# Kernel tuning notes

Hardware: AMD Instinct MI355X
Metric: run time of the kernel (lower is better)

The kernel has to match this reference:

```python
import jax, jax.numpy as jnp
import numpy as np

EPS_BN = 1e-5
EPS_LN = 1e-5
OUT_H, OUT_W = 256, 256


def conv2d(x, w, b, pad):
    y = jax.lax.conv_general_dilated(x, w, (1, 1), [(pad, pad), (pad, pad)],
                                     dimension_numbers=('NCHW', 'OIHW', 'NCHW'))
    return y + b[None, :, None, None]


def leaky(x):
    return jnp.where(x >= 0, x, 0.2 * x)


def bn_eval(x, g, b):
    # fresh BatchNorm2d in eval mode: running_mean=0, running_var=1
    scale = g / jnp.sqrt(1.0 + EPS_BN)
    return x * scale[None, :, None, None] + b[None, :, None, None]


def resize_bilinear(x, oh, ow):
    # align_corners=True bilinear, separable gathers
    n, c, h, w = x.shape
    sy = jnp.arange(oh, dtype=x.dtype) * ((h - 1) / (oh - 1))
    sx = jnp.arange(ow, dtype=x.dtype) * ((w - 1) / (ow - 1))
    y0 = jnp.clip(jnp.floor(sy).astype(jnp.int32), 0, h - 2)
    x0 = jnp.clip(jnp.floor(sx).astype(jnp.int32), 0, w - 2)
    fy = (sy - y0.astype(x.dtype))[None, None, :, None]
    fx = (sx - x0.astype(x.dtype))[None, None, None, :]
    top = x[:, :, y0, :] * (1 - fy) + x[:, :, y0 + 1, :] * fy        # (n,c,oh,w)
    out = top[:, :, :, x0] * (1 - fx) + top[:, :, :, x0 + 1] * fx    # (n,c,oh,ow)
    return out


def layernorm(x, g, b):
    mu = jnp.mean(x, axis=-1, keepdims=True)
    var = jnp.mean((x - mu) ** 2, axis=-1, keepdims=True)
    return (x - mu) * jax.lax.rsqrt(var + EPS_LN) * g + b


def setup_inputs() -> dict:
    key = jax.random.key(0)
    ks = iter(jax.random.split(key, 64))

    def rn(shape, scale=0.05):
        return (jax.random.normal(next(ks), shape, dtype=jnp.float32) * scale)

    inp = {'x': jax.random.normal(next(ks), (8, 64, 128, 128), dtype=jnp.float32)}
    inp.update(
        r_c7a_w=rn((16, 64, 7, 7)), r_c7a_b=jnp.zeros((16,), jnp.float32),
        r_c1_w=rn((16, 16, 1, 1)), r_c1_b=jnp.zeros((16,), jnp.float32),
        r_bn1_g=1.0 + rn((16,), 0.1), r_bn1_b=jnp.zeros((16,), jnp.float32),
        rb_c1_w=rn((16, 16, 3, 3)), rb_c1_b=jnp.zeros((16,), jnp.float32),
        rb_bn1_g=1.0 + rn((16,), 0.1), rb_bn1_b=jnp.zeros((16,), jnp.float32),
        rb_c2_w=rn((16, 16, 3, 3)), rb_c2_b=jnp.zeros((16,), jnp.float32),
        rb_bn2_g=1.0 + rn((16,), 0.1), rb_bn2_b=jnp.zeros((16,), jnp.float32),
        r_c3_w=rn((16, 16, 3, 3)), r_c3_b=jnp.zeros((16,), jnp.float32),
        r_bn2_g=1.0 + rn((16,), 0.1), r_bn2_b=jnp.zeros((16,), jnp.float32),
        r_c7b_w=rn((64, 16, 7, 7)), r_c7b_b=jnp.zeros((64,), jnp.float32),
        a_k_w=rn((1, 64, 1, 1)), a_k_b=jnp.zeros((1,), jnp.float32),
        a_q_w=rn((1, 64, 1, 1)), a_q_b=jnp.zeros((1,), jnp.float32),
        a_v_w=rn((8, 64, 1, 1)), a_v_b=jnp.zeros((8,), jnp.float32),
        a_r_w=rn((64, 8, 1, 1)), a_r_b=jnp.zeros((64,), jnp.float32),
        t_ln_g=jnp.ones((64,), jnp.float32), t_ln_b=jnp.zeros((64,), jnp.float32),
        t_fc1_w=rn((64, 64)), t_fc1_b=jnp.zeros((64,), jnp.float32),
        t_fc2_w=rn((64, 64)), t_fc2_b=jnp.zeros((64,), jnp.float32),
    )
    return inp


def reference(x, r_c7a_w, r_c7a_b, r_c1_w, r_c1_b, r_bn1_g, r_bn1_b,
              rb_c1_w, rb_c1_b, rb_bn1_g, rb_bn1_b, rb_c2_w, rb_c2_b,
              rb_bn2_g, rb_bn2_b, r_c3_w, r_c3_b, r_bn2_g, r_bn2_b,
              r_c7b_w, r_c7b_b, a_k_w, a_k_b, a_q_w, a_q_b, a_v_w, a_v_b,
              a_r_w, a_r_b, t_ln_g, t_ln_b, t_fc1_w, t_fc1_b, t_fc2_w, t_fc2_b):
    # ---- Resizer ----
    identity = resize_bilinear(x, OUT_H, OUT_W)
    y = leaky(conv2d(x, r_c7a_w, r_c7a_b, 3))
    y = bn_eval(leaky(conv2d(y, r_c1_w, r_c1_b, 0)), r_bn1_g, r_bn1_b)
    y = resize_bilinear(y, OUT_H, OUT_W)
    conv_identity = y
    z = leaky(bn_eval(conv2d(y, rb_c1_w, rb_c1_b, 1), rb_bn1_g, rb_bn1_b))
    z = bn_eval(conv2d(z, rb_c2_w, rb_c2_b, 1), rb_bn2_g, rb_bn2_b) + y
    z = bn_eval(conv2d(z, r_c3_w, r_c3_b, 1), r_bn2_g, r_bn2_b) + conv_identity
    out = conv2d(z, r_c7b_w, r_c7b_b, 3) + identity

    # ---- EfficientAttention (key_channels=1, head_count=1, value_channels=8) ----
    n, c, h, w = out.shape
    hw = h * w
    k = conv2d(out, a_k_w, a_k_b, 0).reshape(n, 1, hw)
    q = conv2d(out, a_q_w, a_q_b, 0).reshape(n, 1, hw)
    v = conv2d(out, a_v_w, a_v_b, 0).reshape(n, 8, hw)
    key = jax.nn.softmax(k, axis=2)            # softmax over spatial positions
    query = jax.nn.softmax(q, axis=1)          # size-1 channel axis -> ones (faithful)
    context = jnp.einsum('nkp,nvp->nkv', key, v)          # (n,1,8)
    att = jnp.einsum('nkv,nkp->nvp', context, query)      # (n,8,hw)
    out = conv2d(att.reshape(n, 8, h, w), a_r_w, a_r_b, 0) + out

    # ---- TransformerBlock (identity conv, 1 encoder: x + MLP(LN(x))) ----
    t = out.reshape(n, c, hw).transpose(2, 0, 1)          # (hw, n, c)
    tn = layernorm(t, t_ln_g, t_ln_b)
    m = jax.nn.gelu(tn @ t_fc1_w.T + t_fc1_b, approximate=False) @ t_fc2_w.T + t_fc2_b
    t = t + m
    return t.transpose(1, 2, 0).reshape(n, c, h, w)
```

## Files before the change

kernel.cpp:

```cpp
#include <hip/hip_runtime.h>
#include <math.h>

#define DI __device__ __forceinline__
#define HW128 (128*128)
#define HW256 (256*256)

__device__ const float BN_RS = 0.9999950000374997f;

DI float leakyf(float x){ return x >= 0.f ? x : 0.2f*x; }

DI unsigned short f2bf(float f){
    unsigned u = __float_as_uint(f);
    return (unsigned short)((u + 0x7fffu + ((u >> 16) & 1u)) >> 16);
}
DI void unpack2(unsigned u, float& lo, float& hi){
    lo = __uint_as_float(u << 16);
    hi = __uint_as_float(u & 0xffff0000u);
}
DI void load8(const uint4* s, size_t idx, unsigned* d){
    uint4 t0 = s[idx], t1 = s[idx + 1];
    d[0]=t0.x; d[1]=t0.y; d[2]=t0.z; d[3]=t0.w;
    d[4]=t1.x; d[5]=t1.y; d[6]=t1.z; d[7]=t1.w;
}

typedef __attribute__((ext_vector_type(8))) short short8v;
typedef __attribute__((ext_vector_type(4))) float float4v;

__global__ __launch_bounds__(256) void prepack(
    const float* __restrict__ w7a, const float* __restrict__ w1,
    const float* __restrict__ w3a, const float* __restrict__ b3a, const float* __restrict__ g3a, const float* __restrict__ be3a,
    const float* __restrict__ w3b, const float* __restrict__ b3b, const float* __restrict__ g3b, const float* __restrict__ be3b,
    const float* __restrict__ w3c, const float* __restrict__ b3c, const float* __restrict__ g3c, const float* __restrict__ be3c,
    const float* __restrict__ w7b, const float* __restrict__ fc1w, const float* __restrict__ fc2w,
    unsigned short* __restrict__ p7aB, float* __restrict__ p1,
    float* __restrict__ q3a, float* __restrict__ q3b, float* __restrict__ q3c,
    unsigned short* __restrict__ w3aB, unsigned short* __restrict__ w3bB, unsigned short* __restrict__ w3cB,
    unsigned short* __restrict__ pwB,
    unsigned short* __restrict__ pwT1, unsigned short* __restrict__ pwT2)
{
    int i = blockIdx.x * 256 + threadIdx.x;
    if (i < 57344) {
        int g = i / 14336, rem = i - g*14336;
        int ks = rem >> 9, oc = (rem >> 5) & 15, k = rem & 31;
        int ky = ks >> 2, kx = ((ks & 3) << 1) + (k >> 4), ic = g*16 + (k & 15);
        p7aB[i] = (kx < 7) ? f2bf(w7a[(oc*64 + ic)*49 + ky*7 + kx]) : (unsigned short)0;
    }
    if (i < 57344) {
        int ks = i >> 11, oc = (i >> 5) & 63, k = i & 31;
        int ky = ks >> 2, kx = ((ks & 3) << 1) + (k >> 4), ic = k & 15;
        pwB[i] = (kx < 7) ? f2bf(w7b[((oc*16 + ic)*7 + ky)*7 + kx]) : (unsigned short)0;
    }
    if (i < 3072) {
        int ks = i >> 9, oc = (i >> 5) & 15, k = i & 31;
        int ky = ks >> 1, kx = ((ks & 1) << 1) + (k >> 4), ic = k & 15;
        if (kx < 3) {
            int src = (oc*16 + ic)*9 + ky*3 + kx;
            w3aB[i] = f2bf(w3a[src] * (g3a[oc]*BN_RS));
            w3bB[i] = f2bf(w3b[src] * (g3b[oc]*BN_RS));
            w3cB[i] = f2bf(w3c[src] * (g3c[oc]*BN_RS));
        } else {
            w3aB[i] = 0; w3bB[i] = 0; w3cB[i] = 0;
        }
    }
    if (i < 256) { int oc = i & 15, ic = i >> 4; p1[i] = w1[oc*16 + ic]; }
    if (i < 16) {
        q3a[i] = b3a[i]*(g3a[i]*BN_RS) + be3a[i];
        q3b[i] = b3b[i]*(g3b[i]*BN_RS) + be3b[i];
        q3c[i] = b3c[i]*(g3c[i]*BN_RS) + be3c[i];
    }
    if (i < 4096) { pwT1[i] = f2bf(fc1w[i]); pwT2[i] = f2bf(fc2w[i]); }
}

__global__ __launch_bounds__(256) void x_to_ci(
    const float* __restrict__ x, unsigned short* __restrict__ xci)
{
    int idx = blockIdx.x*256 + threadIdx.x;
    int p = idx & 16383, gn = idx >> 14;
    int g = gn & 3, n = gn >> 2;
    const float* xb = x + (size_t)(n*64 + g*16)*HW128 + p;
    unsigned q[8];
#pragma unroll
    for (int h = 0; h < 8; ++h) {
        float a0 = xb[(size_t)(2*h)*HW128];
        float a1 = xb[(size_t)(2*h + 1)*HW128];
        q[h] = (unsigned)f2bf(a0) | ((unsigned)f2bf(a1) << 16);
    }
    uint4* dst = (uint4*)xci + (size_t)idx*2;
    dst[0] = make_uint4(q[0], q[1], q[2], q[3]);
    dst[1] = make_uint4(q[4], q[5], q[6], q[7]);
}

__global__ __launch_bounds__(256) void conv7a_mfma(
    const unsigned short* __restrict__ xci,
    const unsigned short* __restrict__ pw,
    const float* __restrict__ b7a, const float* __restrict__ p1,
    const float* __restrict__ b1, const float* __restrict__ bng,
    const float* __restrict__ bnb, unsigned short* __restrict__ y2ci)
{
    __shared__ __align__(16) unsigned char lds[17408];
    unsigned short* tile = (unsigned short*)lds;
    float* P16 = (float*)lds;

    const int tid = threadIdx.x;
    const int n = blockIdx.z, ox = blockIdx.x*16, oy = blockIdx.y*16;
    const int w = tid >> 6, l = tid & 63, lg = l >> 4, ln = l & 15;

    float4v acc[4];
#pragma unroll
    for (int mi = 0; mi < 4; ++mi) acc[mi] = (float4v){0.f,0.f,0.f,0.f};

    const uint4* xc4 = (const uint4*)xci;
    uint4* tl4 = (uint4*)tile;
    const short8v* Bb = (const short8v*)pw;

    for (int g = 0; g < 4; ++g) {
        __syncthreads();
        for (int u = tid; u < 1056; u += 256) {
            int r = u / 48, s = u - r*48;
            int y = oy + r - 3, xcol = ox + (s >> 1) - 3;
            uint4 v = make_uint4(0u,0u,0u,0u);
            if (y >= 0 && y < 128 && xcol >= 0 && xcol < 128)
                v = xc4[((size_t)(n*4 + g)*16384 + y*128 + xcol)*2 + (s & 1)];
            tl4[u] = v;
        }
        __syncthreads();
        for (int ks = 0; ks < 28; ++ks) {
            const int ky = ks >> 2, kxp = (ks & 3) << 1;
            short8v b = Bb[(g*28 + ks)*64 + ln*4 + lg];
            short8v a[4];
#pragma unroll
            for (int mi = 0; mi < 4; ++mi) {
                int row = (4*w + mi) + ky;
                a[mi] = *(const short8v*)(tile + (row*24 + ln + kxp)*16 + lg*8);
            }
#pragma unroll
            for (int mi = 0; mi < 4; ++mi)
                acc[mi] = __builtin_amdgcn_mfma_f32_16x16x32_bf16(a[mi], b, acc[mi], 0, 0, 0);
        }
    }
    __syncthreads();
    const float bo = b7a[ln];
#pragma unroll
    for (int mi = 0; mi < 4; ++mi)
#pragma unroll
        for (int r = 0; r < 4; ++r)
            P16[((4*w + mi)*16 + lg*4 + r)*17 + ln] = leakyf(acc[mi][r] + bo);
    __syncthreads();
    const int py = tid >> 4, pxx = tid & 15;
    float lv[16];
#pragma unroll
    for (int ic = 0; ic < 16; ++ic) lv[ic] = P16[tid*17 + ic];
    float u16[16];
#pragma unroll
    for (int o = 0; o < 16; ++o) {
        float u = b1[o];
#pragma unroll
        for (int ic = 0; ic < 16; ++ic) u += lv[ic] * p1[ic*16 + o];
        u = leakyf(u);
        u16[o] = u * (bng[o]*BN_RS) + bnb[o];
    }
    const int p = (oy + py)*128 + ox + pxx;
    unsigned q[8];
#pragma unroll
    for (int h = 0; h < 8; ++h)
        q[h] = (unsigned)f2bf(u16[2*h]) | ((unsigned)f2bf(u16[2*h+1]) << 16);
    uint4* dst = (uint4*)y2ci + (size_t)(n*16384 + p)*2;
    dst[0] = make_uint4(q[0], q[1], q[2], q[3]);
    dst[1] = make_uint4(q[4], q[5], q[6], q[7]);
}

__global__ __launch_bounds__(256) void resize_ci(
    const unsigned short* __restrict__ y2ci, unsigned short* __restrict__ yci)
{
    const int n = blockIdx.z;
    const int ox = blockIdx.x*16 + threadIdx.x;
    const int oy = blockIdx.y*16 + threadIdx.y;
    float sy = oy * (127.f/255.f), sx = ox * (127.f/255.f);
    int y0 = min((int)sy, 126), x0 = min((int)sx, 126);
    float fy = sy - y0, fx = sx - x0;
    const uint4* src = (const uint4*)y2ci;
    size_t i00 = ((size_t)n*16384 + y0*128 + x0)*2;
    unsigned A00[8], A01[8], A10[8], A11[8];
    load8(src, i00,       A00);
    load8(src, i00 + 2,   A01);
    load8(src, i00 + 256, A10);
    load8(src, i00 + 258, A11);
    unsigned q[8];
#pragma unroll
    for (int h = 0; h < 8; ++h) {
        float l00, h00, l01, h01, l10, h10, l11, h11;
        unpack2(A00[h], l00, h00); unpack2(A01[h], l01, h01);
        unpack2(A10[h], l10, h10); unpack2(A11[h], l11, h11);
        float lo = (l00*(1.f-fx) + l01*fx)*(1.f-fy) + (l10*(1.f-fx) + l11*fx)*fy;
        float hi = (h00*(1.f-fx) + h01*fx)*(1.f-fy) + (h10*(1.f-fx) + h11*fx)*fy;
        q[h] = (unsigned)f2bf(lo) | ((unsigned)f2bf(hi) << 16);
    }
    uint4* dst = (uint4*)yci + ((size_t)n*65536 + oy*256 + ox)*2;
    dst[0] = make_uint4(q[0], q[1], q[2], q[3]);
    dst[1] = make_uint4(q[4], q[5], q[6], q[7]);
}

template<int MODE>
__global__ __launch_bounds__(256) void conv3_mfma(
    const unsigned short* __restrict__ in_ci,
    const unsigned short* __restrict__ wB, const float* __restrict__ q3,
    const unsigned short* __restrict__ res_ci,
    unsigned short* __restrict__ out_ci)
{
    __shared__ __align__(16) unsigned char lds[17408];
    unsigned short* tile = (unsigned short*)lds;
    float* P16 = (float*)lds;

    const int tid = threadIdx.x;
    const int n = blockIdx.z, ox = blockIdx.x*16, oy = blockIdx.y*16;
    const int w = tid >> 6, l = tid & 63, lg = l >> 4, ln = l & 15;

    const uint4* zc = (const uint4*)in_ci;
    uint4* tl4 = (uint4*)tile;
    for (int u = tid; u < 720; u += 256) {
        int r = u / 40, s = u - r*40;
        int y = oy + r - 1, xcol = ox + (s >> 1) - 1;
        uint4 v = make_uint4(0u,0u,0u,0u);
        if (y >= 0 && y < 256 && xcol >= 0 && xcol < 256)
            v = zc[((size_t)n*65536 + y*256 + xcol)*2 + (s & 1)];
        tl4[u] = v;
    }
    __syncthreads();

    float4v acc[4];
#pragma unroll
    for (int mi = 0; mi < 4; ++mi) acc[mi] = (float4v){0.f,0.f,0.f,0.f};
    const short8v* Bb = (const short8v*)wB;
#pragma unroll
    for (int ks = 0; ks < 6; ++ks) {
        const int ky = ks >> 1, kxp = (ks & 1) << 1;
        short8v b = Bb[(ks*16 + ln)*4 + lg];
        short8v a[4];
#pragma unroll
        for (int mi = 0; mi < 4; ++mi) {
            int row = (4*w + mi) + ky;
            a[mi] = *(const short8v*)(tile + (row*20 + ln + kxp)*16 + lg*8);
        }
#pragma unroll
        for (int mi = 0; mi < 4; ++mi)
            acc[mi] = __builtin_amdgcn_mfma_f32_16x16x32_bf16(a[mi], b, acc[mi], 0, 0, 0);
    }
    __syncthreads();
#pragma unroll
    for (int mi = 0; mi < 4; ++mi)
#pragma unroll
        for (int r = 0; r < 4; ++r)
            P16[((4*w + mi)*16 + lg*4 + r)*17 + ln] = acc[mi][r];
    __syncthreads();

    const int py = tid >> 4, pxx = tid & 15;
    const int p = (oy + py)*256 + ox + pxx;
    float u16[16];
#pragma unroll
    for (int o = 0; o < 16; ++o) u16[o] = P16[tid*17 + o] + q3[o];
    if (MODE == 0) {
#pragma unroll
        for (int o = 0; o < 16; ++o) u16[o] = leakyf(u16[o]);
    } else {
        unsigned R[8];
        load8((const uint4*)res_ci, ((size_t)n*65536 + p)*2, R);
#pragma unroll
        for (int h = 0; h < 8; ++h) {
            float lo, hi; unpack2(R[h], lo, hi);
            u16[2*h] += lo; u16[2*h+1] += hi;
        }
    }
    unsigned q[8];
#pragma unroll
    for (int h = 0; h < 8; ++h)
        q[h] = (unsigned)f2bf(u16[2*h]) | ((unsigned)f2bf(u16[2*h+1]) << 16);
    uint4* dst = (uint4*)out_ci + ((size_t)n*65536 + p)*2;
    dst[0] = make_uint4(q[0], q[1], q[2], q[3]);
    dst[1] = make_uint4(q[4], q[5], q[6], q[7]);
}

__global__ __launch_bounds__(256) void conv7b_mfma(
    const unsigned short* __restrict__ z_ci,
    const unsigned short* __restrict__ pwB,
    const unsigned short* __restrict__ xci,
    const float* __restrict__ bias,
    const float* __restrict__ akw, const float* __restrict__ akb,
    float* __restrict__ out0, float* __restrict__ kbuf)
{
    __shared__ __align__(16) unsigned char lds[17408 + 14400];
    unsigned short* tile = (unsigned short*)lds;
    float* P16 = (float*)lds;
    unsigned short* xt16 = (unsigned short*)(lds + 17408);

    const int tid = threadIdx.x;
    const int n = blockIdx.z, ox = blockIdx.x*16, oy = blockIdx.y*16;
    const float SC = 127.f/255.f;
    const int ybase = (int)(oy*SC), xbase = (int)(ox*SC);

    const uint4* zc = (const uint4*)z_ci;
    uint4* tl4 = (uint4*)tile;
    for (int u = tid; u < 1056; u += 256) {
        int r = u / 48, s = u - r*48;
        int y = oy + r - 3, xcol = ox + (s >> 1) - 3;
        uint4 v = make_uint4(0u, 0u, 0u, 0u);
        if (y >= 0 && y < 256 && xcol >= 0 && xcol < 256)
            v = zc[(size_t)((n*256 + y)*256 + xcol)*2 + (s & 1)];
        tl4[u] = v;
    }
    const uint4* xc4 = (const uint4*)xci;
    uint4* xt4 = (uint4*)xt16;
    for (int u = tid; u < 900; u += 256) {
        int p = u / 9, s = u - p*9;
        uint4 v = make_uint4(0u, 0u, 0u, 0u);
        if (s < 8) {
            int g = s >> 1, half = s & 1;
            int r = p / 10, c = p - r*10;
            int y = ybase + r, xcc = xbase + c;
            if (y < 128 && xcc < 128)
                v = xc4[((size_t)(n*4 + g)*16384 + y*128 + xcc)*2 + half];
        }
        xt4[u] = v;
    }
    __syncthreads();

    const int w = tid >> 6, l = tid & 63;
    const int lg = l >> 4, ln = l & 15;
    float4v acc[4][4];
#pragma unroll
    for (int mi = 0; mi < 4; ++mi)
#pragma unroll
        for (int nt = 0; nt < 4; ++nt)
            acc[mi][nt] = (float4v){0.f, 0.f, 0.f, 0.f};

    const short8v* Bb = (const short8v*)pwB;
    for (int ks = 0; ks < 28; ++ks) {
        const int ky = ks >> 2, kxp = (ks & 3) << 1;
        short8v a[4], b[4];
#pragma unroll
        for (int mi = 0; mi < 4; ++mi) {
            int row = (4*w + mi) + ky;
            a[mi] = *(const short8v*)(tile + (row*24 + ln + kxp)*16 + lg*8);
        }
#pragma unroll
        for (int nt = 0; nt < 4; ++nt)
            b[nt] = Bb[ks*256 + nt*64 + ln*4 + lg];
#pragma unroll
        for (int mi = 0; mi < 4; ++mi)
#pragma unroll
            for (int nt = 0; nt < 4; ++nt)
                acc[mi][nt] = __builtin_amdgcn_mfma_f32_16x16x32_bf16(
                    a[mi], b[nt], acc[mi][nt], 0, 0, 0);
    }

    const int py = tid >> 4, pxx = tid & 15;
    const int ohy = oy + py, ohx = ox + pxx;
    float sy = ohy*SC, sx = ohx*SC;
    int y0 = min((int)sy, 126), x0 = min((int)sx, 126);
    float fy = sy - y0, fx = sx - x0;
    const int ly = y0 - ybase, lx = x0 - xbase;
    const int p = ohy*256 + ohx;
    const uint4* xt4c = (const uint4*)xt16;
    const size_t q00 = (size_t)(ly*10 + lx)*9;
    float kacc = akb[0];

    for (int nt = 0; nt < 4; ++nt) {
        __syncthreads();
#pragma unroll
        for (int mi = 0; mi < 4; ++mi)
#pragma unroll
            for (int r = 0; r < 4; ++r)
                P16[((4*w + mi)*16 + lg*4 + r)*17 + ln] = acc[mi][nt][r];
        __syncthreads();
        unsigned A00[8], A01[8], A10[8], A11[8];
        size_t qb = q00 + nt*2;
        load8(xt4c, qb,      A00);
        load8(xt4c, qb + 9,  A01);
        load8(xt4c, qb + 90, A10);
        load8(xt4c, qb + 99, A11);
        float u16[16];
#pragma unroll
        for (int h = 0; h < 8; ++h) {
            float l00, h00, l01, h01, l10, h10, l11, h11;
            unpack2(A00[h], l00, h00); unpack2(A01[h], l01, h01);
            unpack2(A10[h], l10, h10); unpack2(A11[h], l11, h11);
            u16[2*h]   = (l00*(1.f-fx) + l01*fx)*(1.f-fy) + (l10*(1.f-fx) + l11*fx)*fy;
            u16[2*h+1] = (h00*(1.f-fx) + h01*fx)*(1.f-fy) + (h10*(1.f-fx) + h11*fx)*fy;
        }
#pragma unroll
        for (int o = 0; o < 16; ++o) {
            int oc = nt*16 + o;
            float u = P16[tid*17 + o] + bias[oc] + u16[o];
            out0[(size_t)(n*64 + oc)*HW256 + p] = u;
            kacc += akw[oc] * u;
        }
    }
    kbuf[n*65536 + p] = kacc;
}

__global__ __launch_bounds__(256) void softmax_part(
    const float* __restrict__ kb, float* __restrict__ pst)
{
    __shared__ float red[4];
    __shared__ float bcast;
    const int pc = blockIdx.x, n = blockIdx.y, tid = threadIdx.x;
    const float* kp = kb + n*65536 + pc*8192;
    float mx = -3.0e38f;
    for (int i = tid; i < 8192; i += 256) mx = fmaxf(mx, kp[i]);
#pragma unroll
    for (int off = 1; off < 64; off <<= 1) mx = fmaxf(mx, __shfl_xor(mx, off));
    int w = tid >> 6, l = tid & 63;
    if (l == 0) red[w] = mx;
    __syncthreads();
    if (tid == 0) bcast = fmaxf(fmaxf(red[0], red[1]), fmaxf(red[2], red[3]));
    __syncthreads();
    float BM = bcast;
    float s = 0.f;
    for (int i = tid; i < 8192; i += 256) s += __expf(kp[i] - BM);
#pragma unroll
    for (int off = 1; off < 64; off <<= 1) s += __shfl_xor(s, off);
    __syncthreads();
    if (l == 0) red[w] = s;
    __syncthreads();
    if (tid == 0) {
        pst[(n*8 + pc)*2]     = BM;
        pst[(n*8 + pc)*2 + 1] = red[0] + red[1] + red[2] + red[3];
    }
}

__global__ __launch_bounds__(64) void softmax_comb(
    const float* __restrict__ pst, float* __restrict__ st)
{
    int tid = threadIdx.x;
    if (tid < 8) {
        int n = tid;
        float MX = -3.0e38f;
        for (int c = 0; c < 8; ++c) MX = fmaxf(MX, pst[(n*8 + c)*2]);
        float S = 0.f;
        for (int c = 0; c < 8; ++c)
            S += pst[(n*8 + c)*2 + 1] * __expf(pst[(n*8 + c)*2] - MX);
        st[n] = MX; st[8 + n] = 1.f / S;
    }
}

__global__ __launch_bounds__(256) void att_wsum(
    const float* __restrict__ out0, const float* __restrict__ kb,
    const float* __restrict__ st, float* __restrict__ Sp)
{
    const int cg = blockIdx.x, pc = blockIdx.y, n = blockIdx.z, c0 = cg*8;
    const float mx = st[n];
    const float* kp = kb + n*65536 + pc*16384;
    const float* base = out0 + (size_t)(n*64 + c0)*HW256 + pc*16384;
    float acc[8];
#pragma unroll
    for (int c = 0; c < 8; ++c) acc[c] = 0.f;
    for (int p = threadIdx.x; p < 16384; p += 256) {
        float e = __expf(kp[p] - mx);
#pragma unroll
        for (int c = 0; c < 8; ++c) acc[c] += e * base[c*HW256 + p];
    }
#pragma unroll
    for (int c = 0; c < 8; ++c)
#pragma unroll
        for (int off = 1; off < 64; off <<= 1) acc[c] += __shfl_xor(acc[c], off);
    __shared__ float red[4][8];
    int w = threadIdx.x >> 6, l = threadIdx.x & 63;
    if (l == 0) {
#pragma unroll
        for (int c = 0; c < 8; ++c) red[w][c] = acc[c];
    }
    __syncthreads();
    if (threadIdx.x < 8)
        Sp[n*256 + pc*64 + c0 + threadIdx.x] =
            red[0][threadIdx.x] + red[1][threadIdx.x] + red[2][threadIdx.x] + red[3][threadIdx.x];
}

__global__ __launch_bounds__(512) void ctx_addc(
    const float* __restrict__ Sp, const float* __restrict__ st,
    const float* __restrict__ avw, const float* __restrict__ avb,
    const float* __restrict__ arw, const float* __restrict__ arb,
    float* __restrict__ addc)
{
    __shared__ float ctx[8][8];
    const int tid = threadIdx.x;
    if (tid < 64) {
        int n = tid >> 3, vc = tid & 7;
        float s = 0.f;
        for (int c = 0; c < 64; ++c) {
            float Sv = Sp[n*256 + c] + Sp[n*256 + 64 + c]
                     + Sp[n*256 + 128 + c] + Sp[n*256 + 192 + c];
            s += avw[vc*64 + c] * Sv;
        }
        ctx[n][vc] = s * st[8 + n] + avb[vc];
    }
    __syncthreads();
    int n = tid >> 6, c = tid & 63;
    float a = arb[c];
#pragma unroll
    for (int vc = 0; vc < 8; ++vc) a += arw[c*8 + vc] * ctx[n][vc];
    addc[n*64 + c] = a;
}

__global__ __launch_bounds__(256) void transformer_mfma(
    float* __restrict__ out0, const float* __restrict__ addc,
    const float* __restrict__ lng, const float* __restrict__ lnb,
    const unsigned short* __restrict__ W1b, const float* __restrict__ fc1b,
    const unsigned short* __restrict__ W2b, const float* __restrict__ fc2b)
{
    __shared__ __align__(16) unsigned char lds[17408 + 9216 + 2048];
    float*          Xt = (float*)lds;
    unsigned short* Xb = (unsigned short*)(lds + 17408);
    unsigned short* Hb = Xb;
    float* ps  = (float*)(lds + 17408 + 9216);
    float* ps2 = ps + 256;

    const int tid = threadIdx.x;
    const int n = blockIdx.x >> 10;
    const int p0 = (blockIdx.x & 1023) << 6;
    const float* ac = addc + n*64;

#pragma unroll
    for (int k = 0; k < 4; ++k) {
        int v = k*256 + tid;
        int c = v >> 4, i4 = (v & 15) << 2;
        float4v q = *(const float4v*)(out0 + (size_t)(n*64 + c)*HW256 + p0 + i4);
        float a = ac[c];
#pragma unroll
        for (int r = 0; r < 4; ++r) q[r] += a;
        *(float4v*)&Xt[c*68 + i4] = q;
    }
    __syncthreads();

    const int token = tid & 63, q = tid >> 6;
    float t16[16];
    {
        float sum = 0.f, sq = 0.f;
#pragma unroll
        for (int e = 0; e < 16; ++e) {
            float v = Xt[(q*16 + e)*68 + token];
            t16[e] = v; sum += v; sq += v*v;
        }
        ps[q*64 + token] = sum; ps2[q*64 + token] = sq;
    }
    __syncthreads();
    {
        float sum = ps[token] + ps[64 + token] + ps[128 + token] + ps[192 + token];
        float sq  = ps2[token] + ps2[64 + token] + ps2[128 + token] + ps2[192 + token];
        float mu = sum * (1.f/64.f);
        float var = fmaxf(sq * (1.f/64.f) - mu*mu, 0.f);
        float rs = rsqrtf(var + 1e-5f);
#pragma unroll
        for (int c8 = 0; c8 < 2; ++c8) {
            short8v pk;
#pragma unroll
            for (int e = 0; e < 8; ++e) {
                int c = q*16 + c8*8 + e;
                pk[e] = (short)f2bf((t16[c8*8 + e] - mu)*rs*lng[c] + lnb[c]);
            }
            *(short8v*)&Xb[token*72 + q*16 + c8*8] = pk;
        }
    }
    __syncthreads();

    const int w = tid >> 6, l = tid & 63, lg = l >> 4, ln = l & 15;

    float4v acc1[4];
#pragma unroll
    for (int nt = 0; nt < 4; ++nt) acc1[nt] = (float4v){0.f,0.f,0.f,0.f};
#pragma unroll
    for (int kk = 0; kk < 2; ++kk) {
        short8v a = *(const short8v*)&Xb[(w*16 + ln)*72 + kk*32 + lg*8];
        short8v b[4];
#pragma unroll
        for (int nt = 0; nt < 4; ++nt)
            b[nt] = *(const short8v*)&W1b[(nt*16 + ln)*64 + kk*32 + lg*8];
#pragma unroll
        for (int nt = 0; nt < 4; ++nt)
            acc1[nt] = __builtin_amdgcn_mfma_f32_16x16x32_bf16(a, b[nt], acc1[nt], 0, 0, 0);
    }
    __syncthreads();
#pragma unroll
    for (int nt = 0; nt < 4; ++nt) {
        int j = nt*16 + ln;
        float bj = fc1b[j];
#pragma unroll
        for (int r = 0; r < 4; ++r) {
            int tok = w*16 + lg*4 + r;
            float m = acc1[nt][r] + bj;
            float g = 0.5f*m*(1.f + erff(m*0.70710678118654752f));
            Hb[tok*72 + j] = f2bf(g);
        }
    }
    __syncthreads();

    float4v acc2[4];
#pragma unroll
    for (int nt = 0; nt < 4; ++nt) acc2[nt] = (float4v){0.f,0.f,0.f,0.f};
#pragma unroll
    for (int kk = 0; kk < 2; ++kk) {
        short8v a = *(const short8v*)&Hb[(w*16 + ln)*72 + kk*32 + lg*8];
        short8v b[4];
#pragma unroll
        for (int nt = 0; nt < 4; ++nt)
            b[nt] = *(const short8v*)&W2b[(nt*16 + ln)*64 + kk*32 + lg*8];
#pragma unroll
        for (int nt = 0; nt < 4; ++nt)
            acc2[nt] = __builtin_amdgcn_mfma_f32_16x16x32_bf16(a, b[nt], acc2[nt], 0, 0, 0);
    }
#pragma unroll
    for (int nt = 0; nt < 4; ++nt) {
        int c = nt*16 + ln;
        int tb = w*16 + lg*4;
        float add = fc2b[c];
        float4v t4 = *(const float4v*)&Xt[c*68 + tb];
        float* dst = out0 + (size_t)(n*64 + c)*HW256 + p0 + tb;
        float4v o;
#pragma unroll
        for (int r = 0; r < 4; ++r) o[r] = t4[r] + acc2[nt][r] + add;
        *(float4v*)dst = o;
    }
}

extern "C" void kernel_launch(void* const* d_in, const int* in_sizes, int n_in,
                              void* d_out, int out_size, void* d_ws, size_t ws_size,
                              hipStream_t stream)
{
    (void)in_sizes; (void)n_in; (void)out_size; (void)ws_size;
    const float* x    = (const float*)d_in[0];
    const float* w7a  = (const float*)d_in[1];
    const float* b7a  = (const float*)d_in[2];
    const float* w1   = (const float*)d_in[3];
    const float* b1   = (const float*)d_in[4];
    const float* g1   = (const float*)d_in[5];
    const float* be1  = (const float*)d_in[6];
    const float* w3a  = (const float*)d_in[7];
    const float* b3a  = (const float*)d_in[8];
    const float* g3a  = (const float*)d_in[9];
    const float* be3a = (const float*)d_in[10];
    const float* w3b  = (const float*)d_in[11];
    const float* b3b  = (const float*)d_in[12];
    const float* g3b  = (const float*)d_in[13];
    const float* be3b = (const float*)d_in[14];
    const float* w3c  = (const float*)d_in[15];
    const float* b3c  = (const float*)d_in[16];
    const float* g3c  = (const float*)d_in[17];
    const float* be3c = (const float*)d_in[18];
    const float* w7b  = (const float*)d_in[19];
    const float* b7b  = (const float*)d_in[20];
    const float* akw  = (const float*)d_in[21];
    const float* akb  = (const float*)d_in[22];
    const float* avw  = (const float*)d_in[25];
    const float* avb  = (const float*)d_in[26];
    const float* arw  = (const float*)d_in[27];
    const float* arb  = (const float*)d_in[28];
    const float* lng  = (const float*)d_in[29];
    const float* lnb  = (const float*)d_in[30];
    const float* fc1w = (const float*)d_in[31];
    const float* fc1b = (const float*)d_in[32];
    const float* fc2w = (const float*)d_in[33];
    const float* fc2b = (const float*)d_in[34];

    float* ws = (float*)d_ws;
    unsigned short* y2ci = (unsigned short*)ws;
    unsigned short* yci  = (unsigned short*)(ws + 1048576);
    unsigned short* z1ci = (unsigned short*)(ws + 1048576 + 4194304);
    unsigned short* z2ci = (unsigned short*)(ws + 1048576 + 2*4194304);
    unsigned short* xci  = (unsigned short*)(ws + 1048576 + 3*4194304);
    float* o_k   = ws + 1048576 + 4*4194304;
    float* o_st  = o_k + 524288;
    float* o_pst = o_st + 64;
    float* o_Sp  = o_pst + 128;
    float* o_ad  = o_Sp + 2048;
    unsigned short* p7aB = (unsigned short*)(o_ad + 512);
    float* p1   = o_ad + 512 + 28672;
    float* q3a  = p1 + 256;
    float* q3b  = q3a + 16;
    float* q3c  = q3b + 16;
    unsigned short* w3aB = (unsigned short*)(q3c + 16);
    unsigned short* w3bB = w3aB + 3072;
    unsigned short* w3cB = w3bB + 3072;
    unsigned short* pwB  = w3cB + 3072;
    unsigned short* pwT1 = pwB + 57344;
    unsigned short* pwT2 = pwT1 + 4096;

    unsigned short* z3ci = z1ci;
    float* out0 = (float*)d_out;

    prepack<<<224, 256, 0, stream>>>(w7a, w1, w3a,b3a,g3a,be3a, w3b,b3b,g3b,be3b,
                                     w3c,b3c,g3c,be3c, w7b, fc1w, fc2w,
                                     p7aB, p1, q3a, q3b, q3c, w3aB, w3bB, w3cB,
                                     pwB, pwT1, pwT2);
    x_to_ci<<<2048, 256, 0, stream>>>(x, xci);
    conv7a_mfma<<<dim3(8,8,8), 256, 0, stream>>>(xci, p7aB, b7a, p1, b1, g1, be1, y2ci);
    resize_ci<<<dim3(16,16,8), dim3(16,16), 0, stream>>>(y2ci, yci);
    conv3_mfma<0><<<dim3(16,16,8), 256, 0, stream>>>(yci,  w3aB, q3a, nullptr, z1ci);
    conv3_mfma<1><<<dim3(16,16,8), 256, 0, stream>>>(z1ci, w3bB, q3b, yci,     z2ci);
    conv3_mfma<1><<<dim3(16,16,8), 256, 0, stream>>>(z2ci, w3cB, q3c, yci,     z3ci);
    conv7b_mfma<<<dim3(16,16,8), 256, 0, stream>>>(z3ci, pwB, xci, b7b, akw, akb, out0, o_k);
    softmax_part<<<dim3(8,8), 256, 0, stream>>>(o_k, o_pst);
    softmax_comb<<<1, 64, 0, stream>>>(o_pst, o_st);
    att_wsum<<<dim3(8,4,8), 256, 0, stream>>>(out0, o_k, o_st, o_Sp);
    ctx_addc<<<1, 512, 0, stream>>>(o_Sp, o_st, avw, avb, arw, arb, o_ad);
    transformer_mfma<<<8192, 256, 0, stream>>>(out0, o_ad, lng, lnb, pwT1, fc1b, pwT2, fc2b);
}
```

Baseline: 325.2 us.

## Store conv7b output as bf16 channel-interleaved intermediate for attention and transformer

conv7b now writes its output as packed bf16 in a per-pixel channel-interleaved layout instead of fp32 NCHW into the final output buffer. att_wsum is reorganised to read this layout, with each thread covering 16 channels over pixel chunks, and ctx_addc gains a reduction over the larger partial-sum array. The transformer kernel loads bf16 tokens into a smaller LDS tile and writes fp32 to the output once. This removes an fp32 write plus two fp32 reads of the 134 MB intermediate, at the cost of bf16 rounding on the residual path.

```diff
diff --git a/kernel.cpp b/kernel.cpp
--- a/kernel.cpp
+++ b/kernel.cpp
@@ -13,6 +13,7 @@
     unsigned u = __float_as_uint(f);
     return (unsigned short)((u + 0x7fffu + ((u >> 16) & 1u)) >> 16);
 }
+DI float bf2f(unsigned short us){ return __uint_as_float((unsigned)us << 16); }
 DI void unpack2(unsigned u, float& lo, float& hi){
     lo = __uint_as_float(u << 16);
     hi = __uint_as_float(u & 0xffff0000u);
@@ -285,7 +286,7 @@
     const unsigned short* __restrict__ xci,
     const float* __restrict__ bias,
     const float* __restrict__ akw, const float* __restrict__ akb,
-    float* __restrict__ out0, float* __restrict__ kbuf)
+    unsigned short* __restrict__ oci, float* __restrict__ kbuf)
 {
     __shared__ __align__(16) unsigned char lds[17408 + 14400];
     unsigned short* tile = (unsigned short*)lds;
@@ -362,6 +363,7 @@
     const uint4* xt4c = (const uint4*)xt16;
     const size_t q00 = (size_t)(ly*10 + lx)*9;
     float kacc = akb[0];
+    uint4* odst = (uint4*)oci + ((size_t)(n*65536 + p))*8;
 
     for (int nt = 0; nt < 4; ++nt) {
         __syncthreads();
@@ -386,13 +388,18 @@
             u16[2*h]   = (l00*(1.f-fx) + l01*fx)*(1.f-fy) + (l10*(1.f-fx) + l11*fx)*fy;
             u16[2*h+1] = (h00*(1.f-fx) + h01*fx)*(1.f-fy) + (h10*(1.f-fx) + h11*fx)*fy;
         }
+        unsigned qpk[8];
 #pragma unroll
         for (int o = 0; o < 16; ++o) {
             int oc = nt*16 + o;
-            float u = P16[tid*17 + o] + bias[oc] + u16[o];
-            out0[(size_t)(n*64 + oc)*HW256 + p] = u;
-            kacc += akw[oc] * u;
-        }
+            u16[o] = P16[tid*17 + o] + bias[oc] + u16[o];
+            kacc += akw[oc] * u16[o];
+        }
+#pragma unroll
+        for (int h = 0; h < 8; ++h)
+            qpk[h] = (unsigned)f2bf(u16[2*h]) | ((unsigned)f2bf(u16[2*h+1]) << 16);
+        odst[nt*2]     = make_uint4(qpk[0], qpk[1], qpk[2], qpk[3]);
+        odst[nt*2 + 1] = make_uint4(qpk[4], qpk[5], qpk[6], qpk[7]);
     }
     kbuf[n*65536 + p] = kacc;
 }
@@ -443,35 +450,46 @@
 }
 
 __global__ __launch_bounds__(256) void att_wsum(
-    const float* __restrict__ out0, const float* __restrict__ kb,
+    const unsigned short* __restrict__ oci, const float* __restrict__ kb,
     const float* __restrict__ st, float* __restrict__ Sp)
 {
-    const int cg = blockIdx.x, pc = blockIdx.y, n = blockIdx.z, c0 = cg*8;
+    const int pc = blockIdx.x, n = blockIdx.y, tid = threadIdx.x;
+    const int qr = tid & 3, pidx0 = tid >> 2;
     const float mx = st[n];
-    const float* kp = kb + n*65536 + pc*16384;
-    const float* base = out0 + (size_t)(n*64 + c0)*HW256 + pc*16384;
-    float acc[8];
-#pragma unroll
-    for (int c = 0; c < 8; ++c) acc[c] = 0.f;
-    for (int p = threadIdx.x; p < 16384; p += 256) {
+    float acc[16];
+#pragma unroll
+    for (int c = 0; c < 16; ++c) acc[c] = 0.f;
+    const float* kp = kb + n*65536 + pc*2048;
+    const uint4* base = (const uint4*)oci + ((size_t)(n*65536 + pc*2048))*8 + qr*2;
+    for (int p = pidx0; p < 2048; p += 64) {
         float e = __expf(kp[p] - mx);
-#pragma unroll
-        for (int c = 0; c < 8; ++c) acc[c] += e * base[c*HW256 + p];
-    }
-#pragma unroll
-    for (int c = 0; c < 8; ++c)
-#pragma unroll
-        for (int off = 1; off < 64; off <<= 1) acc[c] += __shfl_xor(acc[c], off);
-    __shared__ float red[4][8];
-    int w = threadIdx.x >> 6, l = threadIdx.x & 63;
-    if (l == 0) {
-#pragma unroll
-        for (int c = 0; c < 8; ++c) red[w][c] = acc[c];
-    }
-    __syncthreads();
-    if (threadIdx.x < 8)
-        Sp[n*256 + pc*64 + c0 + threadIdx.x] =
-            red[0][threadIdx.x] + red[1][threadIdx.x] + red[2][threadIdx.x] + red[3][threadIdx.x];
+        uint4 t0 = base[(size_t)p*8], t1 = base[(size_t)p*8 + 1];
+        unsigned d[8] = {t0.x, t0.y, t0.z, t0.w, t1.x, t1.y, t1.z, t1.w};
+#pragma unroll
+        for (int h = 0; h < 8; ++h) {
+            float lo, hi; unpack2(d[h], lo, hi);
+            acc[2*h] += e*lo; acc[2*h + 1] += e*hi;
+        }
+    }
+#pragma unroll
+    for (int c = 0; c < 16; ++c) {
+        acc[c] += __shfl_xor(acc[c], 4);
+        acc[c] += __shfl_xor(acc[c], 8);
+        acc[c] += __shfl_xor(acc[c], 16);
+        acc[c] += __shfl_xor(acc[c], 32);
+    }
+    __shared__ float red[4][4][16];
+    int w = tid >> 6, l = tid & 63;
+    if (l < 4) {
+#pragma unroll
+        for (int c = 0; c < 16; ++c) red[w][l][c] = acc[c];
+    }
+    __syncthreads();
+    if (tid < 64) {
+        int q2 = tid >> 4, c = tid & 15;
+        Sp[n*2048 + pc*64 + q2*16 + c] =
+            red[0][q2][c] + red[1][q2][c] + red[2][q2][c] + red[3][q2][c];
+    }
 }
 
 __global__ __launch_bounds__(512) void ctx_addc(
@@ -480,16 +498,20 @@
     const float* __restrict__ arw, const float* __restrict__ arb,
     float* __restrict__ addc)
 {
+    __shared__ float Sf[512];
     __shared__ float ctx[8][8];
     const int tid = threadIdx.x;
+    {
+        int n = tid >> 6, c = tid & 63;
+        float s = 0.f;
+        for (int k = 0; k < 32; ++k) s += Sp[n*2048 + k*64 + c];
+        Sf[n*64 + c] = s;
+    }
+    __syncthreads();
     if (tid < 64) {
         int n = tid >> 3, vc = tid & 7;
         float s = 0.f;
-        for (int c = 0; c < 64; ++c) {
-            float Sv = Sp[n*256 + c] + Sp[n*256 + 64 + c]
-                     + Sp[n*256 + 128 + c] + Sp[n*256 + 192 + c];
-            s += avw[vc*64 + c] * Sv;
-        }
+        for (int c = 0; c < 64; ++c) s += avw[vc*64 + c] * Sf[n*64 + c];
         ctx[n][vc] = s * st[8 + n] + avb[vc];
     }
     __syncthreads();
@@ -501,32 +523,35 @@
 }
 
 __global__ __launch_bounds__(256) void transformer_mfma(
-    float* __restrict__ out0, const float* __restrict__ addc,
+    const unsigned short* __restrict__ oci, float* __restrict__ out,
+    const float* __restrict__ addc,
     const float* __restrict__ lng, const float* __restrict__ lnb,
     const unsigned short* __restrict__ W1b, const float* __restrict__ fc1b,
     const unsigned short* __restrict__ W2b, const float* __restrict__ fc2b)
 {
-    __shared__ __align__(16) unsigned char lds[17408 + 9216 + 2048];
-    float*          Xt = (float*)lds;
-    unsigned short* Xb = (unsigned short*)(lds + 17408);
+    __shared__ __align__(16) unsigned char lds[8448 + 9216 + 2048 + 256];
+    unsigned* Xci = (unsigned*)lds;
+    unsigned short* Xcis = (unsigned short*)lds;
+    unsigned short* Xb = (unsigned short*)(lds + 8448);
     unsigned short* Hb = Xb;
-    float* ps  = (float*)(lds + 17408 + 9216);
+    float* ps  = (float*)(lds + 8448 + 9216);
     float* ps2 = ps + 256;
+    float* ach = ps2 + 256;
 
     const int tid = threadIdx.x;
     const int n = blockIdx.x >> 10;
     const int p0 = (blockIdx.x & 1023) << 6;
-    const float* ac = addc + n*64;
-
-#pragma unroll
-    for (int k = 0; k < 4; ++k) {
+
+    if (tid < 64) ach[tid] = addc[n*64 + tid];
+
+    const uint4* src = (const uint4*)oci + (size_t)(n*65536 + p0)*8;
+#pragma unroll
+    for (int k = 0; k < 2; ++k) {
         int v = k*256 + tid;
-        int c = v >> 4, i4 = (v & 15) << 2;
-        float4v q = *(const float4v*)(out0 + (size_t)(n*64 + c)*HW256 + p0 + i4);
-        float a = ac[c];
-#pragma unroll
-        for (int r = 0; r < 4; ++r) q[r] += a;
-        *(float4v*)&Xt[c*68 + i4] = q;
+        int tok = v >> 3, part = v & 7;
+        uint4 t = src[(size_t)tok*8 + part];
+        unsigned* du = Xci + tok*33 + part*4;
+        du[0] = t.x; du[1] = t.y; du[2] = t.z; du[3] = t.w;
     }
     __syncthreads();
 
@@ -536,7 +561,7 @@
         float sum = 0.f, sq = 0.f;
 #pragma unroll
         for (int e = 0; e < 16; ++e) {
-            float v = Xt[(q*16 + e)*68 + token];
+            float v = bf2f(Xcis[token*66 + q*16 + e]) + ach[q*16 + e];
             t16[e] = v; sum += v; sq += v*v;
         }
         ps[q*64 + token] = sum; ps2[q*64 + token] = sq;
@@ -610,12 +635,12 @@
     for (int nt = 0; nt < 4; ++nt) {
         int c = nt*16 + ln;
         int tb = w*16 + lg*4;
-        float add = fc2b[c];
-        float4v t4 = *(const float4v*)&Xt[c*68 + tb];
-        float* dst = out0 + (size_t)(n*64 + c)*HW256 + p0 + tb;
+        float add = fc2b[c] + ach[c];
+        float* dst = out + (size_t)(n*64 + c)*HW256 + p0 + tb;
         float4v o;
 #pragma unroll
-        for (int r = 0; r < 4; ++r) o[r] = t4[r] + acc2[nt][r] + add;
+        for (int r = 0; r < 4; ++r)
+            o[r] = bf2f(Xcis[(tb + r)*66 + c]) + add + acc2[nt][r];
         *(float4v*)dst = o;
     }
 }
@@ -665,11 +690,12 @@
     unsigned short* z1ci = (unsigned short*)(ws + 1048576 + 4194304);
     unsigned short* z2ci = (unsigned short*)(ws + 1048576 + 2*4194304);
     unsigned short* xci  = (unsigned short*)(ws + 1048576 + 3*4194304);
-    float* o_k   = ws + 1048576 + 4*4194304;
+    unsigned short* oci  = (unsigned short*)(ws + 1048576 + 4*4194304);
+    float* o_k   = ws + 1048576 + 4*4194304 + 16777216;
     float* o_st  = o_k + 524288;
     float* o_pst = o_st + 64;
     float* o_Sp  = o_pst + 128;
-    float* o_ad  = o_Sp + 2048;
+    float* o_ad  = o_Sp + 16384;
     unsigned short* p7aB = (unsigned short*)(o_ad + 512);
     float* p1   = o_ad + 512 + 28672;
     float* q3a  = p1 + 256;
@@ -695,10 +721,10 @@
     conv3_mfma<0><<<dim3(16,16,8), 256, 0, stream>>>(yci,  w3aB, q3a, nullptr, z1ci);
     conv3_mfma<1><<<dim3(16,16,8), 256, 0, stream>>>(z1ci, w3bB, q3b, yci,     z2ci);
     conv3_mfma<1><<<dim3(16,16,8), 256, 0, stream>>>(z2ci, w3cB, q3c, yci,     z3ci);
-    conv7b_mfma<<<dim3(16,16,8), 256, 0, stream>>>(z3ci, pwB, xci, b7b, akw, akb, out0, o_k);
+    conv7b_mfma<<<dim3(16,16,8), 256, 0, stream>>>(z3ci, pwB, xci, b7b, akw, akb, oci, o_k);
     softmax_part<<<dim3(8,8), 256, 0, stream>>>(o_k, o_pst);
     softmax_comb<<<1, 64, 0, stream>>>(o_pst, o_st);
-    att_wsum<<<dim3(8,4,8), 256, 0, stream>>>(out0, o_k, o_st, o_Sp);
+    att_wsum<<<dim3(32,8), 256, 0, stream>>>(oci, o_k, o_st, o_Sp);
     ctx_addc<<<1, 512, 0, stream>>>(o_Sp, o_st, avw, avb, arw, arb, o_ad);
-    transformer_mfma<<<8192, 256, 0, stream>>>(out0, o_ad, lng, lnb, pwT1, fc1b, pwT2, fc2b);
-}
+    transformer_mfma<<<8192, 256, 0, stream>>>(oci, out0, o_ad, lng, lnb, pwT1, fc1b, pwT2, fc2b);
+}
```

New measurement: 311.4 us, median of 2. -4.2%, faster.
